# Optimization experiments

Hardware: AMD Instinct MI355X
Metric: run time of the kernel (lower is better)

Reference implementation:

```python
import jax, jax.numpy as jnp
import numpy as np

D_MODEL = 1024
N_HEADS = 16
D_K = 64
SEQ = 4096
BATCH = 1


def setup_inputs() -> dict:
    key = jax.random.key(0)
    ks = jax.random.split(key, 6)
    s = 1.0 / np.sqrt(D_MODEL)
    return {
        "h": jax.random.normal(ks[0], (BATCH, SEQ, D_MODEL), jnp.float32),
        "gamma": jnp.ones((D_MODEL,), jnp.float32),
        "beta": jnp.zeros((D_MODEL,), jnp.float32),
        "Wq": jax.random.normal(ks[1], (D_MODEL, N_HEADS * D_K), jnp.float32) * s,
        "bq": jnp.zeros((N_HEADS * D_K,), jnp.float32),
        "Wk": jax.random.normal(ks[2], (D_MODEL, N_HEADS * D_K), jnp.float32) * s,
        "bk": jnp.zeros((N_HEADS * D_K,), jnp.float32),
        "Wv": jax.random.normal(ks[3], (D_MODEL, N_HEADS * D_K), jnp.float32) * s,
        "bv": jnp.zeros((N_HEADS * D_K,), jnp.float32),
        "Wo": jax.random.normal(ks[4], (N_HEADS * D_K, D_MODEL), jnp.float32) * s,
        "bo": jnp.zeros((D_MODEL,), jnp.float32),
    }


def _rope(x):
    # x: [b, s, h, d]
    d = x.shape[-1]
    d2 = d // 2
    theta = 1.0 / (10000.0 ** (jnp.arange(0, d, 2, dtype=jnp.float32) / d))  # [d2]
    pos = jnp.arange(x.shape[1], dtype=jnp.float32)  # [s]
    idx_theta = pos[:, None] * theta[None, :]  # [s, d2]
    idx_theta2 = jnp.concatenate([idx_theta, idx_theta], axis=-1)  # [s, d]
    cos = jnp.cos(idx_theta2)[None, :, None, :]
    sin = jnp.sin(idx_theta2)[None, :, None, :]
    neg_half = jnp.concatenate([-x[..., d2:], x[..., :d2]], axis=-1)
    return x * cos + neg_half * sin


def reference(h, gamma, beta, Wq, bq, Wk, bk, Wv, bv, Wo, bo):
    b, s, dm = h.shape
    h_res = h
    # LayerNorm (eps=1e-5, matching torch default)
    mu = jnp.mean(h, axis=-1, keepdims=True)
    var = jnp.var(h, axis=-1, keepdims=True)
    hn = (h - mu) * jax.lax.rsqrt(var + 1e-5) * gamma + beta
    mh = (b, s, N_HEADS, D_K)
    q = (hn @ Wq + bq).reshape(mh)
    k = (hn @ Wk + bk).reshape(mh)
    v = (hn @ Wv + bv).reshape(mh)
    q = _rope(q)
    k = _rope(k)
    scale = 1.0 / np.sqrt(D_K)
    attn = jnp.einsum('bihd,bjhd->bhij', q, k) * scale  # [b,h,s,s]
    # causal mask
    mask = jnp.tril(jnp.ones((s, s), dtype=bool))
    attn = jnp.where(mask, attn, -jnp.inf)
    attn = jax.nn.softmax(attn, axis=-1)
    out = jnp.einsum('bhij,bjhd->bihd', attn, v).reshape(b, s, N_HEADS * D_K)
    return out @ Wo + bo + h_res
```

## Files before the change

kernel.cpp:

```cpp
#include <hip/hip_runtime.h>
#include <stdint.h>

#define SEQLEN 4096
#define DMODEL 1024
#define NHEADS 16
#define DKDIM  64

typedef unsigned short u16;
typedef unsigned int   u32;
using f32x4 = __attribute__((ext_vector_type(4))) float;
using i32x4 = __attribute__((ext_vector_type(4))) int;
using i32x2 = __attribute__((ext_vector_type(2))) int;

__device__ __forceinline__ u16 f2bf(float f) {
    u32 x = __builtin_bit_cast(u32, f);
    u32 r = x + 0x7fffu + ((x >> 16) & 1u);
    return (u16)(r >> 16);
}
__device__ __forceinline__ float exp2a(float x) {
    float r; asm("v_exp_f32 %0, %1" : "=v"(r) : "v"(x)); return r;
}
__device__ __forceinline__ u32 cvtpk(float lo, float hi) {
    u32 r; asm("v_cvt_pk_bf16_f32 %0, %1, %2" : "=v"(r) : "v"(lo), "v"(hi)); return r;
}

__device__ __forceinline__ void mfma_bf16(f32x4& d, i32x4 a, i32x4 b) {
    asm("v_mfma_f32_16x16x32_bf16 %0, %1, %2, %0" : "+v"(d) : "v"(a), "v"(b));
}
__device__ __forceinline__ void mfma16_bf16(f32x4& d, i32x2 a, i32x2 b) {
    asm("v_mfma_f32_16x16x16_bf16 %0, %1, %2, %0" : "+v"(d) : "v"(a), "v"(b));
}

#define ASYNC_COPY16(gsrc, ldst) \
    __builtin_amdgcn_global_load_lds((const __attribute__((address_space(1))) void*)(gsrc), \
                                     (__attribute__((address_space(3))) void*)(ldst), 16, 0, 0)

__global__ __launch_bounds__(256) void ln_kernel(const float* __restrict__ h,
                                                 const float* __restrict__ gamma,
                                                 const float* __restrict__ beta,
                                                 u16* __restrict__ hn) {
    int row = blockIdx.x;
    int t = threadIdx.x;
    float4 v = reinterpret_cast<const float4*>(h + (size_t)row * DMODEL)[t];
    float s  = v.x + v.y + v.z + v.w;
    float s2 = v.x*v.x + v.y*v.y + v.z*v.z + v.w*v.w;
#pragma unroll
    for (int off = 1; off < 64; off <<= 1) {
        s  += __shfl_xor(s, off);
        s2 += __shfl_xor(s2, off);
    }
    __shared__ float red[8];
    int wid = t >> 6, lane = t & 63;
    if (lane == 0) { red[wid] = s; red[4 + wid] = s2; }
    __syncthreads();
    s  = red[0] + red[1] + red[2] + red[3];
    s2 = red[4] + red[5] + red[6] + red[7];
    float mu   = s * (1.0f / DMODEL);
    float rstd = rsqrtf(s2 * (1.0f / DMODEL) - mu * mu + 1e-5f);
    float4 g = reinterpret_cast<const float4*>(gamma)[t];
    float4 b = reinterpret_cast<const float4*>(beta)[t];
    ushort4 o;
    o.x = f2bf((v.x - mu) * rstd * g.x + b.x);
    o.y = f2bf((v.y - mu) * rstd * g.y + b.y);
    o.z = f2bf((v.z - mu) * rstd * g.z + b.z);
    o.w = f2bf((v.w - mu) * rstd * g.w + b.w);
    reinterpret_cast<ushort4*>(hn + (size_t)row * DMODEL)[t] = o;
}

__global__ __launch_bounds__(256) void wconv_kernel(const float* __restrict__ Wq,
                                                    const float* __restrict__ Wk,
                                                    const float* __restrict__ Wv,
                                                    const float* __restrict__ Wo,
                                                    u16* __restrict__ wqkvT,
                                                    u16* __restrict__ woT) {
    int z = blockIdx.z;
    const float* W = (z == 0) ? Wq : (z == 1) ? Wk : (z == 2) ? Wv : Wo;
    u16* Wt = (z < 3) ? wqkvT + (size_t)z * DMODEL * DMODEL : woT;
    __shared__ float tile[32][33];
    int bx = blockIdx.x * 32;
    int by = blockIdx.y * 32;
    int tx = threadIdx.x & 31, ty = threadIdx.x >> 5;
#pragma unroll
    for (int i = 0; i < 32; i += 8)
        tile[ty + i][tx] = W[(size_t)(by + ty + i) * DMODEL + bx + tx];
    __syncthreads();
#pragma unroll
    for (int i = 0; i < 32; i += 8)
        Wt[(size_t)(bx + ty + i) * DMODEL + by + tx] = f2bf(tile[tx][ty + i]);
}

__global__ void rope_table_kernel(float* __restrict__ cosT, float* __restrict__ sinT) {
    int idx = blockIdx.x * 256 + threadIdx.x;
    int s = idx >> 5, i = idx & 31;
    float theta = powf(10000.0f, -2.0f * (float)i / 64.0f);
    float ang = (float)s * theta;
    cosT[idx] = cosf(ang);
    sinT[idx] = sinf(ang);
}

template <int EPI>
__global__ __launch_bounds__(256) void gemm_kernel(const u16* __restrict__ A,
                                                   const u16* __restrict__ Bt,
                                                   const float* __restrict__ b0,
                                                   const float* __restrict__ b1,
                                                   const float* __restrict__ b2,
                                                   const float* __restrict__ resid,
                                                   const float* __restrict__ cosT,
                                                   const float* __restrict__ sinT,
                                                   u16* __restrict__ o0,
                                                   u16* __restrict__ o1,
                                                   u16* __restrict__ o2,
                                                   float* __restrict__ ofp) {
    __shared__ alignas(16) u16 As[2][128 * 64];
    __shared__ alignas(16) u16 Bs[2][128 * 64];
    int bm = blockIdx.x, bn = blockIdx.y;
    int tid = threadIdx.x;
    int wid = tid >> 6, lane = tid & 63;
    int wm = wid >> 1, wn = wid & 1;
    int t15 = lane & 15, g = lane >> 4;
    const u16* Abase = A  + (size_t)bm * 128 * DMODEL;
    const u16* Bbase = Bt + (size_t)bn * 128 * DMODEL;
    int srow = tid >> 3;
    int sslot = tid & 7;
    f32x4 acc[4][4] = {};

#define GSTAGE(b, ks)                                                                    \
    {                                                                                    \
        _Pragma("unroll")                                                                \
        for (int i = 0; i < 4; i++) {                                                    \
            int row = i * 32 + srow;                                                     \
            int col = ((sslot ^ (row & 7)) * 8) + (ks);                                  \
            ASYNC_COPY16(Abase + (size_t)row * DMODEL + col, &As[b][i * 2048 + wid * 512]); \
            ASYNC_COPY16(Bbase + (size_t)row * DMODEL + col, &Bs[b][i * 2048 + wid * 512]); \
        }                                                                                \
    }

    GSTAGE(0, 0)
    __syncthreads();
    int buf = 0;
    for (int ks = 0; ks < DMODEL; ks += 64) {
        if (ks < DMODEL - 64) GSTAGE(buf ^ 1, ks + 64)
#pragma unroll
        for (int kk = 0; kk < 2; kk++) {
            i32x4 af[4], bfr[4];
#pragma unroll
            for (int mi = 0; mi < 4; mi++) {
                int row = wm * 64 + mi * 16 + t15;
                int sl = (kk * 4 + g) ^ (row & 7);
                af[mi] = *reinterpret_cast<const i32x4*>(&As[buf][row * 64 + sl * 8]);
            }
#pragma unroll
            for (int ni = 0; ni < 4; ni++) {
                int row = wn * 64 + ni * 16 + t15;
                int sl = (kk * 4 + g) ^ (row & 7);
                bfr[ni] = *reinterpret_cast<const i32x4*>(&Bs[buf][row * 64 + sl * 8]);
            }
            __builtin_amdgcn_s_setprio(1);
#pragma unroll
            for (int mi = 0; mi < 4; mi++)
#pragma unroll
                for (int ni = 0; ni < 4; ni++)
                    mfma_bf16(acc[mi][ni], af[mi], bfr[ni]);
            __builtin_amdgcn_s_setprio(0);
        }
        __syncthreads();
        buf ^= 1;
    }
#undef GSTAGE

    if (EPI == 0) {
        int seg = bn >> 3;
        int bnl = bn & 7;
        const float* bias = (seg == 0) ? b0 : (seg == 1) ? b1 : b2;
        if (seg < 2) {
            u16* o = (seg == 0) ? o0 : o1;
            float qs = (seg == 0) ? 0.18033688f : 1.0f;
#pragma unroll
            for (int mi = 0; mi < 4; mi++) {
#pragma unroll
                for (int nl = 0; nl < 2; nl++) {
                    int n10 = bnl * 128 + wn * 64 + nl * 16 + t15;
                    int head = n10 >> 6;
                    int dA = n10 & 63, dB = dA + 32;
                    float bvA = bias[n10], bvB = bias[n10 + 32];
#pragma unroll
                    for (int r = 0; r < 4; r++) {
                        int m = bm * 128 + wm * 64 + mi * 16 + g * 4 + r;
                        float c  = cosT[m * 32 + dA];
                        float sn = sinT[m * 32 + dA];
                        float xA = acc[mi][nl][r] + bvA;
                        float xB = acc[mi][nl + 2][r] + bvB;
                        o[(size_t)(head * SEQLEN + m) * DKDIM + dA] = f2bf((xA * c - xB * sn) * qs);
                        o[(size_t)(head * SEQLEN + m) * DKDIM + dB] = f2bf((xB * c + xA * sn) * qs);
                    }
                }
            }
        } else {
#pragma unroll
            for (int mi = 0; mi < 4; mi++) {
#pragma unroll
                for (int ni = 0; ni < 4; ni++) {
                    int n10 = bnl * 128 + wn * 64 + ni * 16 + t15;
                    int head = n10 >> 6, dv = n10 & 63;
                    float bv = bias[n10];
                    int m = bm * 128 + wm * 64 + mi * 16 + g * 4;
                    ushort4 w4;
                    w4.x = f2bf(acc[mi][ni][0] + bv);
                    w4.y = f2bf(acc[mi][ni][1] + bv);
                    w4.z = f2bf(acc[mi][ni][2] + bv);
                    w4.w = f2bf(acc[mi][ni][3] + bv);
                    *reinterpret_cast<ushort4*>(&o2[(size_t)(head * DKDIM + dv) * SEQLEN + m]) = w4;
                }
            }
        }
    } else {
#pragma unroll
        for (int mi = 0; mi < 4; mi++) {
#pragma unroll
            for (int ni = 0; ni < 4; ni++) {
                int n = bn * 128 + wn * 64 + ni * 16 + t15;
                float bv = b0[n];
#pragma unroll
                for (int r = 0; r < 4; r++) {
                    int m = bm * 128 + wm * 64 + mi * 16 + g * 4 + r;
                    ofp[(size_t)m * DMODEL + n] = acc[mi][ni][r] + bv + resid[(size_t)m * DMODEL + n];
                }
            }
        }
    }
}

__global__ __launch_bounds__(256) void attn_kernel(const u16* __restrict__ q,
                                                   const u16* __restrict__ k,
                                                   const u16* __restrict__ vt,
                                                   u16* __restrict__ o) {
    __shared__ alignas(16) u16 Kl[2][64 * 64];
    __shared__ alignas(16) u16 Vl[2][64 * 64];
    int h = blockIdx.y;
    int p = blockIdx.x;
    int tid = threadIdx.x, wid = tid >> 6, lane = tid & 63;
    int t15 = lane & 15, g = lane >> 4;
    const u16* Qh  = q  + (size_t)h * SEQLEN * DKDIM;
    const u16* Kh  = k  + (size_t)h * SEQLEN * DKDIM;
    const u16* VtH = vt + (size_t)h * DKDIM * SEQLEN;
    int sslot = lane & 7;

#define STAGE(b, kt_)                                                                   \
    {                                                                                   \
        int k0s = (kt_) * 64;                                                           \
        _Pragma("unroll")                                                               \
        for (int it = 0; it < 2; it++) {                                                \
            int u   = wid * 2 + it;                                                     \
            int row = u * 8 + (lane >> 3);                                              \
            int sl  = (sslot ^ (row & 7)) * 8;                                          \
            ASYNC_COPY16(Kh + (size_t)(k0s + row) * DKDIM + sl, &Kl[b][u * 512]);       \
            ASYNC_COPY16(VtH + (size_t)row * SEQLEN + k0s + sl, &Vl[b][u * 512]);       \
        }                                                                               \
    }

    for (int pass = 0; pass < 2; pass++) {
        int qt = pass ? p : (63 - p);
        int q0 = qt * 64;
        int qrow = q0 + wid * 16 + t15;
        i32x4 qf0, qf1;
        {
            const u16* qp = Qh + (size_t)qrow * DKDIM + g * 8;
            qf0 = *reinterpret_cast<const i32x4*>(qp);
            qf1 = *reinterpret_cast<const i32x4*>(qp + 32);
        }
        f32x4 oacc[4] = {};
        float m_run = -1e30f, l_part = 0.f;

        STAGE(0, 0)
        __syncthreads();
        int buf = 0;
        for (int kt = 0; kt <= qt; kt++) {
            if (kt < qt) STAGE(buf ^ 1, kt + 1)
            int k0 = kt * 64;
            f32x4 sacc[4] = {};
            __builtin_amdgcn_s_setprio(1);
#pragma unroll
            for (int kb = 0; kb < 4; kb++) {
                int j = kb * 16 + t15;
                i32x4 kf0 = *reinterpret_cast<const i32x4*>(&Kl[buf][j * 64 + ((g ^ (j & 7)) * 8)]);
                i32x4 kf1 = *reinterpret_cast<const i32x4*>(&Kl[buf][j * 64 + (((4 + g) ^ (j & 7)) * 8)]);
                mfma_bf16(sacc[kb], kf0, qf0);
                mfma_bf16(sacc[kb], kf1, qf1);
            }
            __builtin_amdgcn_s_setprio(0);
            if (kt == qt) {
#pragma unroll
                for (int kb = 0; kb < 4; kb++)
#pragma unroll
                    for (int r = 0; r < 4; r++) {
                        int kvg = k0 + kb * 16 + g * 4 + r;
                        if (kvg > qrow) sacc[kb][r] = -1e30f;
                    }
            }
            float a0 = fmaxf(fmaxf(sacc[0][0], sacc[0][1]), fmaxf(sacc[0][2], sacc[0][3]));
            float a1 = fmaxf(fmaxf(sacc[1][0], sacc[1][1]), fmaxf(sacc[1][2], sacc[1][3]));
            float a2 = fmaxf(fmaxf(sacc[2][0], sacc[2][1]), fmaxf(sacc[2][2], sacc[2][3]));
            float a3 = fmaxf(fmaxf(sacc[3][0], sacc[3][1]), fmaxf(sacc[3][2], sacc[3][3]));
            float mx = fmaxf(fmaxf(a0, a1), fmaxf(a2, a3));
            if (!__all(mx <= m_run + 8.0f)) {
                float mrow = fmaxf(mx, __shfl_xor(mx, 16));
                mrow = fmaxf(mrow, __shfl_xor(mrow, 32));
                float mnew = fmaxf(m_run, mrow);
                float fold = exp2a(m_run - mnew);
                m_run = mnew;
                l_part *= fold;
                oacc[0] *= fold; oacc[1] *= fold; oacc[2] *= fold; oacc[3] *= fold;
            }
            float ps = 0.f;
            u32 pw[8];
#pragma unroll
            for (int kb = 0; kb < 4; kb++) {
                float p0 = exp2a(sacc[kb][0] - m_run);
                float p1 = exp2a(sacc[kb][1] - m_run);
                float p2 = exp2a(sacc[kb][2] - m_run);
                float p3 = exp2a(sacc[kb][3] - m_run);
                ps += (p0 + p1) + (p2 + p3);
                pw[kb * 2]     = cvtpk(p0, p1);
                pw[kb * 2 + 1] = cvtpk(p2, p3);
            }
            l_part += ps;
            __builtin_amdgcn_s_setprio(1);
#pragma unroll
            for (int nb = 0; nb < 4; nb++) {
                int d = nb * 16 + t15;
#pragma unroll
                for (int kb = 0; kb < 4; kb++) {
                    i32x2 vf = *reinterpret_cast<const i32x2*>(
                        &Vl[buf][d * 64 + (((kb * 2 + (g >> 1)) ^ (d & 7)) * 8) + (g & 1) * 4]);
                    i32x2 pf = i32x2{(int)pw[kb * 2], (int)pw[kb * 2 + 1]};
                    mfma16_bf16(oacc[nb], vf, pf);
                }
            }
            __builtin_amdgcn_s_setprio(0);
            __syncthreads();
            buf ^= 1;
        }
        float l = l_part;
        l += __shfl_xor(l, 16);
        l += __shfl_xor(l, 32);
        float inv_l = 1.0f / l;
#pragma unroll
        for (int nb = 0; nb < 4; nb++) {
            ushort4 w4;
            w4.x = f2bf(oacc[nb][0] * inv_l);
            w4.y = f2bf(oacc[nb][1] * inv_l);
            w4.z = f2bf(oacc[nb][2] * inv_l);
            w4.w = f2bf(oacc[nb][3] * inv_l);
            *reinterpret_cast<ushort4*>(&o[(size_t)qrow * DMODEL + h * DKDIM + nb * 16 + g * 4]) = w4;
        }
    }
#undef STAGE
}

extern "C" void kernel_launch(void* const* d_in, const int* in_sizes, int n_in,
                              void* d_out, int out_size, void* d_ws, size_t ws_size,
                              hipStream_t stream) {
    const float* h     = (const float*)d_in[0];
    const float* gamma = (const float*)d_in[1];
    const float* beta  = (const float*)d_in[2];
    const float* Wq    = (const float*)d_in[3];
    const float* bq    = (const float*)d_in[4];
    const float* Wk    = (const float*)d_in[5];
    const float* bk    = (const float*)d_in[6];
    const float* Wv    = (const float*)d_in[7];
    const float* bv    = (const float*)d_in[8];
    const float* Wo    = (const float*)d_in[9];
    const float* bo    = (const float*)d_in[10];
    float* out = (float*)d_out;

    char* ws = (char*)d_ws;
    u16* hn     = (u16*)(ws);
    u16* wqkvT  = (u16*)(ws + (8ull  << 20));
    u16* woT    = (u16*)(ws + (14ull << 20));
    u16* qb     = (u16*)(ws + (16ull << 20));
    u16* kbuf   = (u16*)(ws + (24ull << 20));
    u16* vtb    = (u16*)(ws + (32ull << 20));
    float* cosT = (float*)(ws + (40ull << 20));
    float* sinT = (float*)(ws + (40ull << 20) + (512ull << 10));
    u16* attn = hn;

    ln_kernel<<<SEQLEN, 256, 0, stream>>>(h, gamma, beta, hn);
    wconv_kernel<<<dim3(32, 32, 4), 256, 0, stream>>>(Wq, Wk, Wv, Wo, wqkvT, woT);
    rope_table_kernel<<<(SEQLEN * 32) / 256, 256, 0, stream>>>(cosT, sinT);
    gemm_kernel<0><<<dim3(32, 24), 256, 0, stream>>>(hn, wqkvT, bq, bk, bv, nullptr,
                                                     cosT, sinT, qb, kbuf, vtb, nullptr);
    dim3 agrid(32, NHEADS);
    attn_kernel<<<agrid, 256, 0, stream>>>(qb, kbuf, vtb, attn);
    gemm_kernel<1><<<dim3(32, 8), 256, 0, stream>>>(attn, woT, bo, nullptr, nullptr, h,
                                                    nullptr, nullptr, nullptr, nullptr, nullptr, out);
}
```

Measured before the change: 159.3 us.

## Process two 16-row query groups per wave to reuse K/V tiles

Each wave now handles 32 query rows (two 16-row groups A and B) instead of 16, so every K/V tile staged into LDS feeds twice as many MFMAs. The query tile per block grows to 128 rows and the attention grid is halved to 16 blocks per head, keeping the causal pairing of short and long tiles across two passes. This cuts LDS traffic and per-tile synchronisation per unit of work, but doubles the accumulator registers, which may lower occupancy, and leaves only 256 blocks, which may underfill the GPU.

```diff
diff --git a/kernel.cpp b/kernel.cpp
--- a/kernel.cpp
+++ b/kernel.cpp
@@ -259,71 +259,97 @@
     }
 
     for (int pass = 0; pass < 2; pass++) {
-        int qt = pass ? p : (63 - p);
-        int q0 = qt * 64;
-        int qrow = q0 + wid * 16 + t15;
-        i32x4 qf0, qf1;
+        int Q = pass ? p : (31 - p);
+        int q0 = Q * 128;
+        int qrowA = q0 + wid * 32 + t15;
+        int qrowB = qrowA + 16;
+        i32x4 qfA0, qfA1, qfB0, qfB1;
         {
-            const u16* qp = Qh + (size_t)qrow * DKDIM + g * 8;
-            qf0 = *reinterpret_cast<const i32x4*>(qp);
-            qf1 = *reinterpret_cast<const i32x4*>(qp + 32);
-        }
-        f32x4 oacc[4] = {};
-        float m_run = -1e30f, l_part = 0.f;
+            const u16* qp = Qh + (size_t)qrowA * DKDIM + g * 8;
+            qfA0 = *reinterpret_cast<const i32x4*>(qp);
+            qfA1 = *reinterpret_cast<const i32x4*>(qp + 32);
+            const u16* qp2 = qp + 16 * DKDIM;
+            qfB0 = *reinterpret_cast<const i32x4*>(qp2);
+            qfB1 = *reinterpret_cast<const i32x4*>(qp2 + 32);
+        }
+        f32x4 oA[4] = {}, oB[4] = {};
+        float mA = -1e30f, mB = -1e30f, lA = 0.f, lB = 0.f;
 
         STAGE(0, 0)
         __syncthreads();
         int buf = 0;
-        for (int kt = 0; kt <= qt; kt++) {
-            if (kt < qt) STAGE(buf ^ 1, kt + 1)
+        int ktend = 2 * Q + 1;
+        for (int kt = 0; kt <= ktend; kt++) {
+            if (kt < ktend) STAGE(buf ^ 1, kt + 1)
             int k0 = kt * 64;
-            f32x4 sacc[4] = {};
+            f32x4 sA[4] = {}, sB[4] = {};
             __builtin_amdgcn_s_setprio(1);
 #pragma unroll
             for (int kb = 0; kb < 4; kb++) {
                 int j = kb * 16 + t15;
                 i32x4 kf0 = *reinterpret_cast<const i32x4*>(&Kl[buf][j * 64 + ((g ^ (j & 7)) * 8)]);
                 i32x4 kf1 = *reinterpret_cast<const i32x4*>(&Kl[buf][j * 64 + (((4 + g) ^ (j & 7)) * 8)]);
-                mfma_bf16(sacc[kb], kf0, qf0);
-                mfma_bf16(sacc[kb], kf1, qf1);
+                mfma_bf16(sA[kb], kf0, qfA0);
+                mfma_bf16(sA[kb], kf1, qfA1);
+                mfma_bf16(sB[kb], kf0, qfB0);
+                mfma_bf16(sB[kb], kf1, qfB1);
             }
             __builtin_amdgcn_s_setprio(0);
-            if (kt == qt) {
+            if (kt >= 2 * Q) {
 #pragma unroll
                 for (int kb = 0; kb < 4; kb++)
 #pragma unroll
                     for (int r = 0; r < 4; r++) {
                         int kvg = k0 + kb * 16 + g * 4 + r;
-                        if (kvg > qrow) sacc[kb][r] = -1e30f;
+                        if (kvg > qrowA) sA[kb][r] = -1e30f;
+                        if (kvg > qrowB) sB[kb][r] = -1e30f;
                     }
             }
-            float a0 = fmaxf(fmaxf(sacc[0][0], sacc[0][1]), fmaxf(sacc[0][2], sacc[0][3]));
-            float a1 = fmaxf(fmaxf(sacc[1][0], sacc[1][1]), fmaxf(sacc[1][2], sacc[1][3]));
-            float a2 = fmaxf(fmaxf(sacc[2][0], sacc[2][1]), fmaxf(sacc[2][2], sacc[2][3]));
-            float a3 = fmaxf(fmaxf(sacc[3][0], sacc[3][1]), fmaxf(sacc[3][2], sacc[3][3]));
-            float mx = fmaxf(fmaxf(a0, a1), fmaxf(a2, a3));
-            if (!__all(mx <= m_run + 8.0f)) {
-                float mrow = fmaxf(mx, __shfl_xor(mx, 16));
-                mrow = fmaxf(mrow, __shfl_xor(mrow, 32));
-                float mnew = fmaxf(m_run, mrow);
-                float fold = exp2a(m_run - mnew);
-                m_run = mnew;
-                l_part *= fold;
-                oacc[0] *= fold; oacc[1] *= fold; oacc[2] *= fold; oacc[3] *= fold;
-            }
-            float ps = 0.f;
-            u32 pw[8];
+            float a0 = fmaxf(fmaxf(sA[0][0], sA[0][1]), fmaxf(sA[0][2], sA[0][3]));
+            float a1 = fmaxf(fmaxf(sA[1][0], sA[1][1]), fmaxf(sA[1][2], sA[1][3]));
+            float a2 = fmaxf(fmaxf(sA[2][0], sA[2][1]), fmaxf(sA[2][2], sA[2][3]));
+            float a3 = fmaxf(fmaxf(sA[3][0], sA[3][1]), fmaxf(sA[3][2], sA[3][3]));
+            float mxA = fmaxf(fmaxf(a0, a1), fmaxf(a2, a3));
+            float b0_ = fmaxf(fmaxf(sB[0][0], sB[0][1]), fmaxf(sB[0][2], sB[0][3]));
+            float b1_ = fmaxf(fmaxf(sB[1][0], sB[1][1]), fmaxf(sB[1][2], sB[1][3]));
+            float b2_ = fmaxf(fmaxf(sB[2][0], sB[2][1]), fmaxf(sB[2][2], sB[2][3]));
+            float b3_ = fmaxf(fmaxf(sB[3][0], sB[3][1]), fmaxf(sB[3][2], sB[3][3]));
+            float mxB = fmaxf(fmaxf(b0_, b1_), fmaxf(b2_, b3_));
+            if (!__all((mxA <= mA + 8.0f) && (mxB <= mB + 8.0f))) {
+                float mrA = fmaxf(mxA, __shfl_xor(mxA, 16));
+                mrA = fmaxf(mrA, __shfl_xor(mrA, 32));
+                float mnA = fmaxf(mA, mrA);
+                float fdA = exp2a(mA - mnA);
+                mA = mnA; lA *= fdA;
+                oA[0] *= fdA; oA[1] *= fdA; oA[2] *= fdA; oA[3] *= fdA;
+                float mrB = fmaxf(mxB, __shfl_xor(mxB, 16));
+                mrB = fmaxf(mrB, __shfl_xor(mrB, 32));
+                float mnB = fmaxf(mB, mrB);
+                float fdB = exp2a(mB - mnB);
+                mB = mnB; lB *= fdB;
+                oB[0] *= fdB; oB[1] *= fdB; oB[2] *= fdB; oB[3] *= fdB;
+            }
+            float psA = 0.f, psB = 0.f;
+            u32 pwA[8], pwB[8];
 #pragma unroll
             for (int kb = 0; kb < 4; kb++) {
-                float p0 = exp2a(sacc[kb][0] - m_run);
-                float p1 = exp2a(sacc[kb][1] - m_run);
-                float p2 = exp2a(sacc[kb][2] - m_run);
-                float p3 = exp2a(sacc[kb][3] - m_run);
-                ps += (p0 + p1) + (p2 + p3);
-                pw[kb * 2]     = cvtpk(p0, p1);
-                pw[kb * 2 + 1] = cvtpk(p2, p3);
-            }
-            l_part += ps;
+                float pa0 = exp2a(sA[kb][0] - mA);
+                float pa1 = exp2a(sA[kb][1] - mA);
+                float pa2 = exp2a(sA[kb][2] - mA);
+                float pa3 = exp2a(sA[kb][3] - mA);
+                psA += (pa0 + pa1) + (pa2 + pa3);
+                pwA[kb * 2]     = cvtpk(pa0, pa1);
+                pwA[kb * 2 + 1] = cvtpk(pa2, pa3);
+                float pb0 = exp2a(sB[kb][0] - mB);
+                float pb1 = exp2a(sB[kb][1] - mB);
+                float pb2 = exp2a(sB[kb][2] - mB);
+                float pb3 = exp2a(sB[kb][3] - mB);
+                psB += (pb0 + pb1) + (pb2 + pb3);
+                pwB[kb * 2]     = cvtpk(pb0, pb1);
+                pwB[kb * 2 + 1] = cvtpk(pb2, pb3);
+            }
+            lA += psA;
+            lB += psB;
             __builtin_amdgcn_s_setprio(1);
 #pragma unroll
             for (int nb = 0; nb < 4; nb++) {
@@ -332,26 +358,35 @@
                 for (int kb = 0; kb < 4; kb++) {
                     i32x2 vf = *reinterpret_cast<const i32x2*>(
                         &Vl[buf][d * 64 + (((kb * 2 + (g >> 1)) ^ (d & 7)) * 8) + (g & 1) * 4]);
-                    i32x2 pf = i32x2{(int)pw[kb * 2], (int)pw[kb * 2 + 1]};
-                    mfma16_bf16(oacc[nb], vf, pf);
+                    mfma16_bf16(oA[nb], vf, i32x2{(int)pwA[kb * 2], (int)pwA[kb * 2 + 1]});
+                    mfma16_bf16(oB[nb], vf, i32x2{(int)pwB[kb * 2], (int)pwB[kb * 2 + 1]});
                 }
             }
             __builtin_amdgcn_s_setprio(0);
             __syncthreads();
             buf ^= 1;
         }
-        float l = l_part;
-        l += __shfl_xor(l, 16);
-        l += __shfl_xor(l, 32);
-        float inv_l = 1.0f / l;
+        float l0 = lA;
+        l0 += __shfl_xor(l0, 16);
+        l0 += __shfl_xor(l0, 32);
+        float invA = 1.0f / l0;
+        float l1 = lB;
+        l1 += __shfl_xor(l1, 16);
+        l1 += __shfl_xor(l1, 32);
+        float invB = 1.0f / l1;
 #pragma unroll
         for (int nb = 0; nb < 4; nb++) {
             ushort4 w4;
-            w4.x = f2bf(oacc[nb][0] * inv_l);
-            w4.y = f2bf(oacc[nb][1] * inv_l);
-            w4.z = f2bf(oacc[nb][2] * inv_l);
-            w4.w = f2bf(oacc[nb][3] * inv_l);
-            *reinterpret_cast<ushort4*>(&o[(size_t)qrow * DMODEL + h * DKDIM + nb * 16 + g * 4]) = w4;
+            w4.x = f2bf(oA[nb][0] * invA);
+            w4.y = f2bf(oA[nb][1] * invA);
+            w4.z = f2bf(oA[nb][2] * invA);
+            w4.w = f2bf(oA[nb][3] * invA);
+            *reinterpret_cast<ushort4*>(&o[(size_t)qrowA * DMODEL + h * DKDIM + nb * 16 + g * 4]) = w4;
+            w4.x = f2bf(oB[nb][0] * invB);
+            w4.y = f2bf(oB[nb][1] * invB);
+            w4.z = f2bf(oB[nb][2] * invB);
+            w4.w = f2bf(oB[nb][3] * invB);
+            *reinterpret_cast<ushort4*>(&o[(size_t)qrowB * DMODEL + h * DKDIM + nb * 16 + g * 4]) = w4;
         }
     }
 #undef STAGE
@@ -389,7 +424,7 @@
     rope_table_kernel<<<(SEQLEN * 32) / 256, 256, 0, stream>>>(cosT, sinT);
     gemm_kernel<0><<<dim3(32, 24), 256, 0, stream>>>(hn, wqkvT, bq, bk, bv, nullptr,
                                                      cosT, sinT, qb, kbuf, vtb, nullptr);
-    dim3 agrid(32, NHEADS);
+    dim3 agrid(16, NHEADS);
     attn_kernel<<<agrid, 256, 0, stream>>>(qb, kbuf, vtb, attn);
     gemm_kernel<1><<<dim3(32, 8), 256, 0, stream>>>(attn, woT, bo, nullptr, nullptr, h,
                                                     nullptr, nullptr, nullptr, nullptr, nullptr, out);
```

Result: slower. 179.5 us (+12.7%).
